# Optimization experiments

Measured on AMD Instinct MI355X. Metric: run time of the kernel, lower is better.

Reference implementation:

```python
import jax, jax.numpy as jnp
import numpy as np

IN_CH = 128
OUT_CH = 1
N_NODES = 20000
N_EDGES = 640000
EPS = 1e-5


def setup_inputs() -> dict:
    key = jax.random.key(0)
    ks = jax.random.split(key, 8)
    x = jax.random.normal(ks[0], (N_NODES, IN_CH), dtype=jnp.float32)
    edge_index = jax.random.randint(ks[1], (2, N_EDGES), 0, N_NODES, dtype=jnp.int64)
    s1 = 1.0 / np.sqrt(2 * IN_CH)
    s2 = 1.0 / np.sqrt(IN_CH)
    return {
        "x": x,
        "edge_index": edge_index,
        "W1": jax.random.normal(ks[2], (2 * IN_CH, IN_CH), dtype=jnp.float32) * s1,
        "b1": jnp.zeros((IN_CH,), dtype=jnp.float32),
        "bn_g": jnp.ones((IN_CH,), dtype=jnp.float32),
        "bn_b": jnp.zeros((IN_CH,), dtype=jnp.float32),
        "W2": jax.random.normal(ks[3], (IN_CH, IN_CH), dtype=jnp.float32) * s2,
        "b2": jnp.zeros((IN_CH,), dtype=jnp.float32),
        "ln_g": jnp.ones((IN_CH,), dtype=jnp.float32),
        "ln_b": jnp.zeros((IN_CH,), dtype=jnp.float32),
        "W3": jax.random.normal(ks[4], (IN_CH, OUT_CH), dtype=jnp.float32) * s2,
        "b3": jnp.zeros((OUT_CH,), dtype=jnp.float32),
    }


def gcn_conv(h, src, dst, num_nodes, bias):
    # h: [num_nodes, F] already linearly transformed. GCN norm with self loops:
    # deg[i] = 1 + in-degree(i); norm_e = deg[src]^-1/2 * deg[dst]^-1/2
    deg = jnp.zeros((num_nodes,), h.dtype).at[dst].add(1.0) + 1.0
    dinv = deg ** -0.5
    norm = dinv[src] * dinv[dst]                      # [E]
    agg = jnp.zeros_like(h).at[dst].add(h[src] * norm[:, None])
    agg = agg + h * (dinv * dinv)[:, None]            # self-loop contribution
    return agg + bias


def reference(x, edge_index, W1, b1, bn_g, bn_b, W2, b2, ln_g, ln_b, W3, b3):
    src, dst = edge_index[0], edge_index[1]
    E = src.shape[0]
    # edge features: [E, 2*IN_CH]
    ef = jnp.concatenate([x[src], x[dst]], axis=1)
    # GCNConv 1 over E "nodes" (edge-feature rows)
    h = gcn_conv(ef @ W1, src, dst, E, b1)
    # BatchNorm1d (training-mode batch stats, biased variance)
    mean = h.mean(axis=0)
    var = h.var(axis=0)
    h = (h - mean) * jax.lax.rsqrt(var + EPS) * bn_g + bn_b
    h = jax.nn.relu(h)
    # GCNConv 2
    h = gcn_conv(h @ W2, src, dst, E, b2)
    # LayerNorm over feature dim
    mu = h.mean(axis=-1, keepdims=True)
    v = h.var(axis=-1, keepdims=True)
    h = (h - mu) * jax.lax.rsqrt(v + EPS) * ln_g + ln_b
    h = jax.nn.relu(h)
    out = h @ W3 + b3                                  # [E, 1]
    return out.squeeze()
```

## Files before the change

kernel.cpp:

```cpp
#include <hip/hip_runtime.h>
#include <hip/hip_bf16.h>

#define NN 20000
#define NE 640000
#define TAILN (NE - NN)
#define F  128
#define EPSN 1e-5f

typedef __bf16 bf16;
typedef bf16  bf16x8 __attribute__((ext_vector_type(8)));
typedef bf16  bf16x4 __attribute__((ext_vector_type(4)));
typedef float f32x4  __attribute__((ext_vector_type(4)));
typedef unsigned short u16;

__global__ void k_cvt_idx(const void* __restrict__ ei_raw, int* __restrict__ srcb,
                          int* __restrict__ dstb, int* __restrict__ cnt,
                          int* __restrict__ cst, int* __restrict__ cdt) {
  const int* e32 = (const int*)ei_raw;
  const long long* e64 = (const long long*)ei_raw;
  bool is64 = true;
#pragma unroll
  for (int k = 0; k < 8; ++k) is64 = is64 && (e32[2 * k + 1] == 0);
  int e = blockIdx.x * 256 + threadIdx.x;
  if (e < NE) {
    int s, d;
    if (is64) { s = (int)e64[e]; d = (int)e64[NE + e]; }
    else      { s = e32[e];      d = e32[NE + e]; }
    srcb[e] = s; dstb[e] = d;
    atomicAdd(&cnt[d], 1);
    if (e >= NN) { atomicAdd(&cst[s], 1); atomicAdd(&cdt[d], 1); }
  }
}

__global__ __launch_bounds__(256) void k1_gemm1(const float* __restrict__ x,
        const float* __restrict__ W1, bf16* __restrict__ xa, bf16* __restrict__ xb) {
  __shared__ float XT[64][129];
  int row0 = blockIdx.x * 64;
  int half = blockIdx.y >> 1;
  int cb   = (blockIdx.y & 1) * 64;
  const float* W = W1 + (size_t)half * F * F;
  bf16* out = half ? xb : xa;
  int t = threadIdx.x;
#pragma unroll
  for (int i = 0; i < 8; ++i) {
    int flat = i * 1024 + t * 4;
    int r = flat >> 7, c = flat & 127;
    int gr = row0 + r;
    f32x4 v = {0.f, 0.f, 0.f, 0.f};
    if (gr < NN) v = *(const f32x4*)(x + (size_t)gr * F + c);
    XT[r][c] = v[0]; XT[r][c + 1] = v[1]; XT[r][c + 2] = v[2]; XT[r][c + 3] = v[3];
  }
  __syncthreads();
  int tc = t & 15, tr = t >> 4;
  float acc[4][4] = {};
  for (int k = 0; k < F; ++k) {
    f32x4 wv = *(const f32x4*)(W + (size_t)k * F + cb + tc * 4);
    float x0 = XT[tr * 4 + 0][k], x1 = XT[tr * 4 + 1][k];
    float x2 = XT[tr * 4 + 2][k], x3 = XT[tr * 4 + 3][k];
#pragma unroll
    for (int j = 0; j < 4; ++j) {
      acc[0][j] += x0 * wv[j]; acc[1][j] += x1 * wv[j];
      acc[2][j] += x2 * wv[j]; acc[3][j] += x3 * wv[j];
    }
  }
#pragma unroll
  for (int i = 0; i < 4; ++i) {
    int gr = row0 + tr * 4 + i;
    if (gr < NN) {
      bf16x4 o;
#pragma unroll
      for (int j = 0; j < 4; ++j) o[j] = (bf16)acc[i][j];
      *(bf16x4*)(out + (size_t)gr * F + cb + tc * 4) = o;
    }
  }
}

__global__ __launch_bounds__(1024) void k3_scan(const int* __restrict__ cnt,
        int* __restrict__ ptr, int* __restrict__ cursor,
        float* __restrict__ dinv, float* __restrict__ invdeg) {
  __shared__ int wsum[16];
  __shared__ int carry_s;
  int t = threadIdx.x;
  int lane = t & 63, wv = t >> 6;
  if (t == 0) carry_s = 0;
  __syncthreads();
  for (int c0 = 0; c0 < NN; c0 += 1024) {
    int i = c0 + t;
    int v = (i < NN) ? cnt[i] : 0;
    int s = v;
#pragma unroll
    for (int off = 1; off < 64; off <<= 1) {
      int n = __shfl_up(s, off);
      if (lane >= off) s += n;
    }
    if (lane == 63) wsum[wv] = s;
    __syncthreads();
    int carry = carry_s;
    int wbase = 0;
#pragma unroll
    for (int k2 = 0; k2 < 16; ++k2) wbase += (k2 < wv) ? wsum[k2] : 0;
    int incl = s + wbase;
    if (i < NN) {
      int excl = carry + incl - v;
      ptr[i] = excl; cursor[i] = excl;
      float deg = (float)(v + 1);
      dinv[i] = rsqrtf(deg);
      invdeg[i] = 1.0f / deg;
    }
    __syncthreads();
    if (t == 1023) carry_s = carry + incl;
    __syncthreads();
  }
  if (t == 0) ptr[NN] = carry_s;
}

__global__ __launch_bounds__(256) void kB_fused(const int* __restrict__ srcb,
        const int* __restrict__ dstb, const bf16* __restrict__ xa,
        const bf16* __restrict__ xb, bf16* __restrict__ hx,
        int* __restrict__ cursor, int* __restrict__ csr_s) {
  int bid = blockIdx.x;
  int t = threadIdx.x;
  if (bid < 2500) {
    int flat = bid * 256 + t;
    int j = flat >> 5, ch = flat & 31;
    if (j >= NN) return;
    if (ch < 16) {
      int s = srcb[j], d = dstb[j];
      bf16x8 a = *(const bf16x8*)(xa + (size_t)s * F + ch * 8);
      bf16x8 b = *(const bf16x8*)(xb + (size_t)d * F + ch * 8);
      bf16x8 o;
#pragma unroll
      for (int m = 0; m < 8; ++m) o[m] = (bf16)((float)a[m] + (float)b[m]);
      *(bf16x8*)(hx + (size_t)j * 256 + ch * 8) = o;
    } else {
      int c8 = (ch - 16) * 8;
      bf16x8 a = *(const bf16x8*)(xa + (size_t)j * F + c8);
      *(bf16x8*)(hx + (size_t)j * 256 + 128 + c8) = a;
    }
  } else {
    int e = (bid - 2500) * 256 + t;
    if (e < NE) {
      int d = dstb[e];
      int pos = atomicAdd(&cursor[d], 1);
      csr_s[pos] = srcb[e] | ((e >= NN) ? (1 << 16) : 0);
    }
  }
}

__global__ __launch_bounds__(256) void k6_conv1cross(const int* __restrict__ ptr,
        const int* __restrict__ csr_s, const bf16* __restrict__ hx,
        const bf16* __restrict__ xb,
        const float* __restrict__ dinv, const float* __restrict__ invdeg,
        const float* __restrict__ b1, float* __restrict__ h1h,
        float* __restrict__ crossrow) {
  int w = threadIdx.x >> 6, lane = threadIdx.x & 63;
  int g = lane >> 4, k = lane & 15;
  int i = blockIdx.x * 4 + w;
  int c0 = k * 8;
  int beg = ptr[i], end = ptr[i + 1];
  float acc[8] = {0,0,0,0,0,0,0,0}, z[8] = {0,0,0,0,0,0,0,0};
  int q = beg + g;
  for (; q + 4 < end; q += 8) {
    int v0 = csr_s[q], v1 = csr_s[q + 4];
    int s0 = v0 & 0xFFFF, s1 = v1 & 0xFFFF;
    float f0 = (v0 >> 16) ? 1.f : 0.f, f1 = (v1 >> 16) ? 1.f : 0.f;
    float d0 = dinv[s0], d1 = dinv[s1];
    const bf16* r0 = hx + (size_t)s0 * 256 + c0;
    const bf16* r1 = hx + (size_t)s1 * 256 + c0;
    bf16x8 h0 = *(const bf16x8*)r0;
    bf16x8 x0 = *(const bf16x8*)(r0 + 128);
    bf16x8 h1 = *(const bf16x8*)r1;
    bf16x8 x1 = *(const bf16x8*)(r1 + 128);
#pragma unroll
    for (int j = 0; j < 8; ++j) {
      acc[j] += d0 * (float)h0[j] + d1 * (float)h1[j];
      z[j]   += f0 * (float)x0[j] + f1 * (float)x1[j];
    }
  }
  if (q < end) {
    int v0 = csr_s[q];
    int s0 = v0 & 0xFFFF;
    float f0 = (v0 >> 16) ? 1.f : 0.f;
    float d0 = dinv[s0];
    const bf16* r0 = hx + (size_t)s0 * 256 + c0;
    bf16x8 h0 = *(const bf16x8*)r0;
    bf16x8 x0 = *(const bf16x8*)(r0 + 128);
#pragma unroll
    for (int j = 0; j < 8; ++j) {
      acc[j] += d0 * (float)h0[j];
      z[j]   += f0 * (float)x0[j];
    }
  }
#pragma unroll
  for (int m = 16; m < 64; m <<= 1) {
#pragma unroll
    for (int j = 0; j < 8; ++j) {
      acc[j] += __shfl_xor(acc[j], m);
      z[j]   += __shfl_xor(z[j], m);
    }
  }
  if (g == 0) {
    float di = dinv[i], iv = invdeg[i];
    bf16x8 self = *(const bf16x8*)(hx + (size_t)i * 256 + c0);
    f32x4 bA = *(const f32x4*)(b1 + c0), bB = *(const f32x4*)(b1 + c0 + 4);
    f32x4 o0, o1;
#pragma unroll
    for (int j = 0; j < 4; ++j) {
      o0[j] = di * acc[j]     + (float)self[j]     * iv + bA[j];
      o1[j] = di * acc[j + 4] + (float)self[j + 4] * iv + bB[j];
    }
    *(f32x4*)(h1h + (size_t)i * F + c0) = o0;
    *(f32x4*)(h1h + (size_t)i * F + c0 + 4) = o1;
  } else if (g == 1) {
    bf16x8 xbv = *(const bf16x8*)(xb + (size_t)i * F + c0);
    f32x4 o0, o1;
#pragma unroll
    for (int j = 0; j < 4; ++j) {
      o0[j] = (float)xbv[j]     * z[j];
      o1[j] = (float)xbv[j + 4] * z[j + 4];
    }
    *(f32x4*)(crossrow + (size_t)i * F + c0) = o0;
    *(f32x4*)(crossrow + (size_t)i * F + c0 + 4) = o1;
  }
}

__global__ __launch_bounds__(256) void k7sr(const float* __restrict__ h1h,
        const float* __restrict__ crossrow, const bf16* __restrict__ xa,
        const bf16* __restrict__ xb, const int* __restrict__ cst,
        const int* __restrict__ cdt, float* __restrict__ statsB) {
  int t = threadIdx.x;
  int w = t >> 6, lane = t & 63, k = lane & 15;
  int rg = t >> 4;
  int c0 = k * 8;
  int base = blockIdx.x * 200;
  float A1[8] = {0,0,0,0,0,0,0,0}, A2[8] = {0,0,0,0,0,0,0,0};
  float B1[8] = {0,0,0,0,0,0,0,0}, B2[8] = {0,0,0,0,0,0,0,0};
  float Cc[8] = {0,0,0,0,0,0,0,0};
  for (int r = rg; r < 200; r += 16) {
    int n = base + r;
    f32x4 h0 = *(const f32x4*)(h1h + (size_t)n * F + c0);
    f32x4 h1 = *(const f32x4*)(h1h + (size_t)n * F + c0 + 4);
    f32x4 cr0 = *(const f32x4*)(crossrow + (size_t)n * F + c0);
    f32x4 cr1 = *(const f32x4*)(crossrow + (size_t)n * F + c0 + 4);
    bf16x8 av = *(const bf16x8*)(xa + (size_t)n * F + c0);
    bf16x8 bv = *(const bf16x8*)(xb + (size_t)n * F + c0);
    float ca = (float)cst[n], cb = (float)cdt[n];
#pragma unroll
    for (int j = 0; j < 4; ++j) {
      A1[j] += h0[j]; A2[j] += h0[j] * h0[j];
      A1[j + 4] += h1[j]; A2[j + 4] += h1[j] * h1[j];
      Cc[j] += cr0[j]; Cc[j + 4] += cr1[j];
    }
#pragma unroll
    for (int j = 0; j < 8; ++j) {
      float a = (float)av[j], b = (float)bv[j];
      B1[j] += ca * a + cb * b;
      B2[j] += ca * a * a + cb * b * b;
    }
  }
#pragma unroll
  for (int m = 16; m < 64; m <<= 1) {
#pragma unroll
    for (int j = 0; j < 8; ++j) {
      A1[j] += __shfl_xor(A1[j], m); A2[j] += __shfl_xor(A2[j], m);
      B1[j] += __shfl_xor(B1[j], m); B2[j] += __shfl_xor(B2[j], m);
      Cc[j] += __shfl_xor(Cc[j], m);
    }
  }
  __shared__ float L[4][5][128];
  if (lane < 16) {
#pragma unroll
    for (int j = 0; j < 8; ++j) {
      L[w][0][c0 + j] = A1[j]; L[w][1][c0 + j] = A2[j];
      L[w][2][c0 + j] = B1[j]; L[w][3][c0 + j] = B2[j];
      L[w][4][c0 + j] = Cc[j];
    }
  }
  __syncthreads();
  if (t < 128) {
#pragma unroll
    for (int term = 0; term < 5; ++term) {
      float v = L[0][term][t] + L[1][term][t] + L[2][term][t] + L[3][term][t];
      atomicAdd(&statsB[term * 128 + t], v);
    }
  }
}

__global__ __launch_bounds__(256) void k8_final(const float* __restrict__ statsB,
        const float* __restrict__ bn_g, const float* __restrict__ bn_b,
        const float* __restrict__ b1, const float* __restrict__ W2,
        const float* __restrict__ b2, const float* __restrict__ lng,
        const float* __restrict__ lnb, const float* __restrict__ W3,
        float* __restrict__ P, float* __restrict__ Qh, float* __restrict__ Qt,
        u16* __restrict__ W2t, f32x4* __restrict__ params4) {
  int t = threadIdx.x;
  if (t < 128) {
    float A1 = statsB[t], A2 = statsB[128 + t], B1v = statsB[256 + t];
    float B2v = statsB[384 + t], Cv = statsB[512 + t];
    float b1c = b1[t];
    float S = A1 + B1v + (float)TAILN * b1c;
    float Q = A2 + B2v + 2.f * Cv + 2.f * b1c * B1v + (float)TAILN * b1c * b1c;
    float mean = S * (1.0f / NE);
    float var = Q * (1.0f / NE) - mean * mean;
    float rs = rsqrtf(var + EPSN);
    float p = bn_g[t] * rs;
    float sh = bn_b[t] - mean * p;
    P[t] = p; Qh[t] = sh; Qt[t] = p * b1c + sh;
    f32x4 pr = {b2[t], lng[t], lnb[t], W3[t]};
    params4[t] = pr;
  }
  for (int i = 0; i < 64; ++i) {
    int flat = i * 256 + t;
    int k = flat >> 7, c = flat & 127;
    union { bf16 b; u16 u; } cv;
    cv.b = (bf16)W2[(size_t)k * F + c];
    W2t[(size_t)c * F + k] = cv.u;
  }
}

__global__ __launch_bounds__(256) void k9a_headgemm(const float* __restrict__ h1h,
        const float* __restrict__ P, const float* __restrict__ Qh,
        const u16* __restrict__ W2t, bf16* __restrict__ h2ph) {
  __shared__ __align__(16) bf16 A[64 * 128];
  __shared__ __align__(16) bf16 B[128 * 128];
  int t = threadIdx.x;
  int row0 = blockIdx.x * 64;
  const bf16x8* srcB = (const bf16x8*)W2t;
#pragma unroll
  for (int i = 0; i < 8; ++i) {
    int ch = i * 256 + t;
    int r = ch >> 4, cir = ch & 15;
    *(bf16x8*)&B[r * 128 + ((cir ^ (r & 7)) << 3)] = srcB[ch];
  }
  {
    int r = t >> 2, sub = t & 3;
    int gr = row0 + r;
#pragma unroll
    for (int j = 0; j < 4; ++j) {
      int c0 = sub * 32 + j * 8;
      f32x4 v0 = {0.f,0.f,0.f,0.f}, v1 = {0.f,0.f,0.f,0.f};
      if (gr < NN) {
        v0 = *(const f32x4*)(h1h + (size_t)gr * F + c0);
        v1 = *(const f32x4*)(h1h + (size_t)gr * F + c0 + 4);
      }
      f32x4 p0 = *(const f32x4*)(P + c0), p1 = *(const f32x4*)(P + c0 + 4);
      f32x4 q0 = *(const f32x4*)(Qh + c0), q1 = *(const f32x4*)(Qh + c0 + 4);
      bf16x8 o;
#pragma unroll
      for (int m = 0; m < 4; ++m) {
        o[m]     = (bf16)fmaxf(v0[m] * p0[m] + q0[m], 0.f);
        o[m + 4] = (bf16)fmaxf(v1[m] * p1[m] + q1[m], 0.f);
      }
      int ch = c0 >> 3;
      *(bf16x8*)&A[r * 128 + ((ch ^ (r & 7)) << 3)] = o;
    }
  }
  __syncthreads();
  int lane = t & 63, w = t >> 6;
  int lr = lane & 15, g = lane >> 4;
  int arow = w * 16 + lr;
  bf16x8 af[4];
#pragma unroll
  for (int kk = 0; kk < 4; ++kk)
    af[kk] = *(const bf16x8*)&A[arow * 128 + (((kk * 4 + g) ^ (arow & 7)) << 3)];
  f32x4 acc[8];
#pragma unroll
  for (int n = 0; n < 8; ++n) {
    f32x4 a = {0.f,0.f,0.f,0.f};
    int col = n * 16 + lr;
#pragma unroll
    for (int kk = 0; kk < 4; ++kk) {
      bf16x8 bfr = *(const bf16x8*)&B[col * 128 + (((kk * 4 + g) ^ (col & 7)) << 3)];
      a = __builtin_amdgcn_mfma_f32_16x16x32_bf16(af[kk], bfr, a, 0, 0, 0);
    }
    acc[n] = a;
  }
#pragma unroll
  for (int n = 0; n < 8; ++n) {
#pragma unroll
    for (int r4 = 0; r4 < 4; ++r4) {
      int gr = row0 + w * 16 + g * 4 + r4;
      if (gr < NN) h2ph[(size_t)gr * F + n * 16 + lr] = (bf16)acc[n][r4];
    }
  }
}

__global__ __launch_bounds__(256) void k9b_head(const int* __restrict__ ptr,
        const int* __restrict__ csr_s, const bf16* __restrict__ h2ph,
        const float* __restrict__ dinv, const float* __restrict__ invdeg,
        const float* __restrict__ b2, const float* __restrict__ lng,
        const float* __restrict__ lnb, const float* __restrict__ W3,
        const float* __restrict__ b3, float* __restrict__ out) {
  int w = threadIdx.x >> 6, lane = threadIdx.x & 63;
  int g = lane >> 4, k = lane & 15;
  int i = blockIdx.x * 4 + w;
  int c0 = k * 8;
  int beg = ptr[i], end = ptr[i + 1];
  float acc[8] = {0,0,0,0,0,0,0,0};
  int q = beg + g;
  for (; q + 4 < end; q += 8) {
    int s0 = csr_s[q] & 0xFFFF, s1 = csr_s[q + 4] & 0xFFFF;
    float d0 = dinv[s0], d1 = dinv[s1];
    bf16x8 h0 = *(const bf16x8*)(h2ph + (size_t)s0 * F + c0);
    bf16x8 h1 = *(const bf16x8*)(h2ph + (size_t)s1 * F + c0);
#pragma unroll
    for (int j = 0; j < 8; ++j)
      acc[j] += d0 * (float)h0[j] + d1 * (float)h1[j];
  }
  if (q < end) {
    int s0 = csr_s[q] & 0xFFFF;
    float d0 = dinv[s0];
    bf16x8 h0 = *(const bf16x8*)(h2ph + (size_t)s0 * F + c0);
#pragma unroll
    for (int j = 0; j < 8; ++j) acc[j] += d0 * (float)h0[j];
  }
#pragma unroll
  for (int m = 16; m < 64; m <<= 1) {
#pragma unroll
    for (int j = 0; j < 8; ++j) acc[j] += __shfl_xor(acc[j], m);
  }
  float di = dinv[i], iv = invdeg[i];
  bf16x8 self = *(const bf16x8*)(h2ph + (size_t)i * F + c0);
  f32x4 b2A = *(const f32x4*)(b2 + c0), b2B = *(const f32x4*)(b2 + c0 + 4);
  float h2[8];
#pragma unroll
  for (int j = 0; j < 4; ++j) {
    h2[j]     = di * acc[j]     + (float)self[j]     * iv + b2A[j];
    h2[j + 4] = di * acc[j + 4] + (float)self[j + 4] * iv + b2B[j];
  }
  float s1v = 0.f, s2v = 0.f;
#pragma unroll
  for (int j = 0; j < 8; ++j) { s1v += h2[j]; s2v += h2[j] * h2[j]; }
#pragma unroll
  for (int m = 1; m < 16; m <<= 1) { s1v += __shfl_xor(s1v, m); s2v += __shfl_xor(s2v, m); }
  float mean = s1v * (1.0f / F);
  float var = s2v * (1.0f / F) - mean * mean;
  float rs = rsqrtf(var + EPSN);
  f32x4 lgA = *(const f32x4*)(lng + c0), lgB = *(const f32x4*)(lng + c0 + 4);
  f32x4 lbA = *(const f32x4*)(lnb + c0), lbB = *(const f32x4*)(lnb + c0 + 4);
  f32x4 w3A = *(const f32x4*)(W3 + c0),  w3B = *(const f32x4*)(W3 + c0 + 4);
  float y = 0.f;
#pragma unroll
  for (int j = 0; j < 4; ++j) {
    y += fmaxf((h2[j]     - mean) * rs * lgA[j] + lbA[j], 0.f) * w3A[j];
    y += fmaxf((h2[j + 4] - mean) * rs * lgB[j] + lbB[j], 0.f) * w3B[j];
  }
#pragma unroll
  for (int m = 1; m < 16; m <<= 1) y += __shfl_xor(y, m);
  if (lane == 0) out[i] = y + b3[0];
}

__global__ __launch_bounds__(256) void k9c_tail(const int* __restrict__ srcb,
        const int* __restrict__ dstb, const bf16* __restrict__ xa,
        const bf16* __restrict__ xb, const float* __restrict__ P,
        const float* __restrict__ Qt, const u16* __restrict__ W2t,
        const f32x4* __restrict__ params4, const float* __restrict__ b3,
        float* __restrict__ out) {
  __shared__ __align__(16) bf16 B[128 * 128];
  int t = threadIdx.x;
  const bf16x8* srcB = (const bf16x8*)W2t;
#pragma unroll
  for (int i = 0; i < 8; ++i) {
    int ch = i * 256 + t;
    int r = ch >> 4, cir = ch & 15;
    *(bf16x8*)&B[r * 128 + ((cir ^ (r & 7)) << 3)] = srcB[ch];
  }
  __syncthreads();
  int lane = t & 63, w = t >> 6;
  int lr = lane & 15, g = lane >> 4;
  int ebase = NN + blockIdx.x * 256 + w * 64;
  float b3v = b3[0];
  for (int rc = 0; rc < 4; ++rc) {
    int e = ebase + rc * 16 + lr;
    bool ok = (e < NE);
    int se = 0, de = 0;
    if (ok) { se = srcb[e]; de = dstb[e]; }
    bf16x8 af[4];
#pragma unroll
    for (int kk = 0; kk < 4; ++kk) {
      int c0 = kk * 32 + g * 8;
      bf16x8 o;
      if (ok) {
        bf16x8 av = *(const bf16x8*)(xa + (size_t)se * F + c0);
        bf16x8 bv = *(const bf16x8*)(xb + (size_t)de * F + c0);
        f32x4 p0 = *(const f32x4*)(P + c0), p1 = *(const f32x4*)(P + c0 + 4);
        f32x4 q0 = *(const f32x4*)(Qt + c0), q1 = *(const f32x4*)(Qt + c0 + 4);
#pragma unroll
        for (int m = 0; m < 4; ++m) {
          o[m]     = (bf16)fmaxf(((float)av[m] + (float)bv[m]) * p0[m] + q0[m], 0.f);
          o[m + 4] = (bf16)fmaxf(((float)av[m + 4] + (float)bv[m + 4]) * p1[m] + q1[m], 0.f);
        }
      } else {
#pragma unroll
        for (int m = 0; m < 8; ++m) o[m] = (bf16)0.f;
      }
      af[kk] = o;
    }
    f32x4 acc[8];
#pragma unroll
    for (int n = 0; n < 8; ++n) {
      f32x4 a = {0.f,0.f,0.f,0.f};
      int col = n * 16 + lr;
#pragma unroll
      for (int kk = 0; kk < 4; ++kk) {
        bf16x8 bfr = *(const bf16x8*)&B[col * 128 + (((kk * 4 + g) ^ (col & 7)) << 3)];
        a = __builtin_amdgcn_mfma_f32_16x16x32_bf16(af[kk], bfr, a, 0, 0, 0);
      }
      acc[n] = a;
    }
#pragma unroll
    for (int r4 = 0; r4 < 4; ++r4) {
      float vv[8];
      float s = 0.f, q = 0.f;
#pragma unroll
      for (int n = 0; n < 8; ++n) {
        float v = acc[n][r4] + params4[n * 16 + lr][0];
        vv[n] = v; s += v; q += v * v;
      }
#pragma unroll
      for (int m = 1; m < 16; m <<= 1) { s += __shfl_xor(s, m); q += __shfl_xor(q, m); }
      float mean = s * (1.0f / F);
      float var = q * (1.0f / F) - mean * mean;
      float rs = rsqrtf(var + EPSN);
      float o = 0.f;
#pragma unroll
      for (int n = 0; n < 8; ++n) {
        f32x4 pr = params4[n * 16 + lr];
        o += fmaxf((vv[n] - mean) * rs * pr[1] + pr[2], 0.f) * pr[3];
      }
#pragma unroll
      for (int m = 1; m < 16; m <<= 1) o += __shfl_xor(o, m);
      int eo = ebase + rc * 16 + g * 4 + r4;
      if (lr == 0 && eo < NE) out[eo] = o + b3v;
    }
  }
}

extern "C" void kernel_launch(void* const* d_in, const int* in_sizes, int n_in,
                              void* d_out, int out_size, void* d_ws, size_t ws_size,
                              hipStream_t stream) {
  const float* x   = (const float*)d_in[0];
  const void*  ei  = d_in[1];
  const float* W1  = (const float*)d_in[2];
  const float* b1  = (const float*)d_in[3];
  const float* bng = (const float*)d_in[4];
  const float* bnb = (const float*)d_in[5];
  const float* W2  = (const float*)d_in[6];
  const float* b2  = (const float*)d_in[7];
  const float* lng = (const float*)d_in[8];
  const float* lnb = (const float*)d_in[9];
  const float* W3  = (const float*)d_in[10];
  const float* b3  = (const float*)d_in[11];
  float* out = (float*)d_out;

  char* ws = (char*)d_ws;
  size_t off = 0;
  auto alloc = [&](size_t bytes) -> char* {
    off = (off + 511) & ~(size_t)511;
    char* p = ws + off;
    off += bytes;
    return p;
  };
  const size_t NFh = (size_t)NN * F * 2;
  bf16*  xa     = (bf16*)alloc(NFh);
  bf16*  xb     = (bf16*)alloc(NFh);
  bf16*  hx     = (bf16*)alloc((size_t)NN * 256 * 2);
  float* h1h    = (float*)alloc((size_t)NN * F * 4);
  float* crossr = (float*)alloc((size_t)NN * F * 4);
  int*   srcb   = (int*)alloc((size_t)NE * 4);
  int*   dstb   = (int*)alloc((size_t)NE * 4);
  int*   csr_s  = (int*)alloc((size_t)NE * 4);
  int*   cnt    = (int*)alloc((size_t)NN * 4);
  int*   cst    = (int*)alloc((size_t)NN * 4);
  int*   cdt    = (int*)alloc((size_t)NN * 4);
  int*   ptrb   = (int*)alloc((size_t)(NN + 1) * 4);
  int*   cursor = (int*)alloc((size_t)NN * 4);
  float* dinv   = (float*)alloc((size_t)NN * 4);
  float* invdeg = (float*)alloc((size_t)NN * 4);
  float* statsB = (float*)alloc(5 * 128 * 4);
  float* Pp     = (float*)alloc(128 * 4);
  float* Qh     = (float*)alloc(128 * 4);
  float* Qt     = (float*)alloc(128 * 4);
  u16*   W2t    = (u16*)alloc((size_t)F * F * 2);
  f32x4* params4= (f32x4*)alloc(128 * 16);
  bf16*  h2ph   = hx;

  hipMemsetAsync(cnt, 0, (size_t)NN * 4, stream);
  hipMemsetAsync(cst, 0, (size_t)NN * 4, stream);
  hipMemsetAsync(cdt, 0, (size_t)NN * 4, stream);
  hipMemsetAsync(statsB, 0, 5 * 128 * 4, stream);

  k_cvt_idx<<<2500, 256, 0, stream>>>(ei, srcb, dstb, cnt, cst, cdt);
  k1_gemm1<<<dim3(313, 4), 256, 0, stream>>>(x, W1, xa, xb);
  k3_scan<<<1, 1024, 0, stream>>>(cnt, ptrb, cursor, dinv, invdeg);
  kB_fused<<<5000, 256, 0, stream>>>(srcb, dstb, xa, xb, hx, cursor, csr_s);
  k6_conv1cross<<<5000, 256, 0, stream>>>(ptrb, csr_s, hx, xb, dinv, invdeg, b1,
                                          h1h, crossr);
  k7sr<<<100, 256, 0, stream>>>(h1h, crossr, xa, xb, cst, cdt, statsB);
  k8_final<<<1, 256, 0, stream>>>(statsB, bng, bnb, b1, W2, b2, lng, lnb, W3,
                                  Pp, Qh, Qt, W2t, params4);
  k9a_headgemm<<<313, 256, 0, stream>>>(h1h, Pp, Qh, W2t, h2ph);
  k9b_head<<<5000, 256, 0, stream>>>(ptrb, csr_s, h2ph, dinv, invdeg, b2, lng, lnb,
                                     W3, b3, out);
  k9c_tail<<<2422, 256, 0, stream>>>(srcb, dstb, xa, xb, Pp, Qt, W2t, params4,
                                     b3, out);
}
```

Before: 459.5 us.

## Prescale rows by dinv and fuse head aggregation with tail kernel

Multiplies each source row by dinv when hx and g2 are written, so the aggregation loops no longer gather dinv[s] per edge and the self-loop term collapses to di*(acc+self). The k9b head aggregation and k9c tail MFMA kernels are merged into one launch that branches on block index, so the two independent workloads can run concurrently and one launch disappears. In exchange, the prescaled values are rounded to bf16 after scaling, which changes the numerics slightly. Tail blocks now carry the extra parameter and register footprint of the fused kernel, and a launch-bounds occupancy hint is added.

```diff
diff --git a/kernel.cpp b/kernel.cpp
--- a/kernel.cpp
+++ b/kernel.cpp
@@ -116,8 +116,8 @@
 
 __global__ __launch_bounds__(256) void kB_fused(const int* __restrict__ srcb,
         const int* __restrict__ dstb, const bf16* __restrict__ xa,
-        const bf16* __restrict__ xb, bf16* __restrict__ hx,
-        int* __restrict__ cursor, int* __restrict__ csr_s) {
+        const bf16* __restrict__ xb, const float* __restrict__ dinv,
+        bf16* __restrict__ hx, int* __restrict__ cursor, int* __restrict__ csr_s) {
   int bid = blockIdx.x;
   int t = threadIdx.x;
   if (bid < 2500) {
@@ -126,11 +126,12 @@
     if (j >= NN) return;
     if (ch < 16) {
       int s = srcb[j], d = dstb[j];
+      float dj = dinv[j];
       bf16x8 a = *(const bf16x8*)(xa + (size_t)s * F + ch * 8);
       bf16x8 b = *(const bf16x8*)(xb + (size_t)d * F + ch * 8);
       bf16x8 o;
 #pragma unroll
-      for (int m = 0; m < 8; ++m) o[m] = (bf16)((float)a[m] + (float)b[m]);
+      for (int m = 0; m < 8; ++m) o[m] = (bf16)(dj * ((float)a[m] + (float)b[m]));
       *(bf16x8*)(hx + (size_t)j * 256 + ch * 8) = o;
     } else {
       int c8 = (ch - 16) * 8;
@@ -150,7 +151,7 @@
 __global__ __launch_bounds__(256) void k6_conv1cross(const int* __restrict__ ptr,
         const int* __restrict__ csr_s, const bf16* __restrict__ hx,
         const bf16* __restrict__ xb,
-        const float* __restrict__ dinv, const float* __restrict__ invdeg,
+        const float* __restrict__ dinv,
         const float* __restrict__ b1, float* __restrict__ h1h,
         float* __restrict__ crossrow) {
   int w = threadIdx.x >> 6, lane = threadIdx.x & 63;
@@ -164,7 +165,6 @@
     int v0 = csr_s[q], v1 = csr_s[q + 4];
     int s0 = v0 & 0xFFFF, s1 = v1 & 0xFFFF;
     float f0 = (v0 >> 16) ? 1.f : 0.f, f1 = (v1 >> 16) ? 1.f : 0.f;
-    float d0 = dinv[s0], d1 = dinv[s1];
     const bf16* r0 = hx + (size_t)s0 * 256 + c0;
     const bf16* r1 = hx + (size_t)s1 * 256 + c0;
     bf16x8 h0 = *(const bf16x8*)r0;
@@ -173,7 +173,7 @@
     bf16x8 x1 = *(const bf16x8*)(r1 + 128);
 #pragma unroll
     for (int j = 0; j < 8; ++j) {
-      acc[j] += d0 * (float)h0[j] + d1 * (float)h1[j];
+      acc[j] += (float)h0[j] + (float)h1[j];
       z[j]   += f0 * (float)x0[j] + f1 * (float)x1[j];
     }
   }
@@ -181,13 +181,12 @@
     int v0 = csr_s[q];
     int s0 = v0 & 0xFFFF;
     float f0 = (v0 >> 16) ? 1.f : 0.f;
-    float d0 = dinv[s0];
     const bf16* r0 = hx + (size_t)s0 * 256 + c0;
     bf16x8 h0 = *(const bf16x8*)r0;
     bf16x8 x0 = *(const bf16x8*)(r0 + 128);
 #pragma unroll
     for (int j = 0; j < 8; ++j) {
-      acc[j] += d0 * (float)h0[j];
+      acc[j] += (float)h0[j];
       z[j]   += f0 * (float)x0[j];
     }
   }
@@ -200,14 +199,14 @@
     }
   }
   if (g == 0) {
-    float di = dinv[i], iv = invdeg[i];
+    float di = dinv[i];
     bf16x8 self = *(const bf16x8*)(hx + (size_t)i * 256 + c0);
     f32x4 bA = *(const f32x4*)(b1 + c0), bB = *(const f32x4*)(b1 + c0 + 4);
     f32x4 o0, o1;
 #pragma unroll
     for (int j = 0; j < 4; ++j) {
-      o0[j] = di * acc[j]     + (float)self[j]     * iv + bA[j];
-      o1[j] = di * acc[j + 4] + (float)self[j + 4] * iv + bB[j];
+      o0[j] = di * (acc[j]     + (float)self[j])     + bA[j];
+      o1[j] = di * (acc[j + 4] + (float)self[j + 4]) + bB[j];
     }
     *(f32x4*)(h1h + (size_t)i * F + c0) = o0;
     *(f32x4*)(h1h + (size_t)i * F + c0 + 4) = o1;
@@ -320,7 +319,8 @@
 
 __global__ __launch_bounds__(256) void k9a_headgemm(const float* __restrict__ h1h,
         const float* __restrict__ P, const float* __restrict__ Qh,
-        const u16* __restrict__ W2t, bf16* __restrict__ h2ph) {
+        const u16* __restrict__ W2t, const float* __restrict__ dinv,
+        bf16* __restrict__ g2) {
   __shared__ __align__(16) bf16 A[64 * 128];
   __shared__ __align__(16) bf16 B[128 * 128];
   int t = threadIdx.x;
@@ -376,163 +376,162 @@
     acc[n] = a;
   }
 #pragma unroll
-  for (int n = 0; n < 8; ++n) {
-#pragma unroll
-    for (int r4 = 0; r4 < 4; ++r4) {
-      int gr = row0 + w * 16 + g * 4 + r4;
-      if (gr < NN) h2ph[(size_t)gr * F + n * 16 + lr] = (bf16)acc[n][r4];
-    }
-  }
-}
-
-__global__ __launch_bounds__(256) void k9b_head(const int* __restrict__ ptr,
-        const int* __restrict__ csr_s, const bf16* __restrict__ h2ph,
-        const float* __restrict__ dinv, const float* __restrict__ invdeg,
-        const float* __restrict__ b2, const float* __restrict__ lng,
-        const float* __restrict__ lnb, const float* __restrict__ W3,
-        const float* __restrict__ b3, float* __restrict__ out) {
-  int w = threadIdx.x >> 6, lane = threadIdx.x & 63;
-  int g = lane >> 4, k = lane & 15;
-  int i = blockIdx.x * 4 + w;
-  int c0 = k * 8;
-  int beg = ptr[i], end = ptr[i + 1];
-  float acc[8] = {0,0,0,0,0,0,0,0};
-  int q = beg + g;
-  for (; q + 4 < end; q += 8) {
-    int s0 = csr_s[q] & 0xFFFF, s1 = csr_s[q + 4] & 0xFFFF;
-    float d0 = dinv[s0], d1 = dinv[s1];
-    bf16x8 h0 = *(const bf16x8*)(h2ph + (size_t)s0 * F + c0);
-    bf16x8 h1 = *(const bf16x8*)(h2ph + (size_t)s1 * F + c0);
-#pragma unroll
-    for (int j = 0; j < 8; ++j)
-      acc[j] += d0 * (float)h0[j] + d1 * (float)h1[j];
-  }
-  if (q < end) {
-    int s0 = csr_s[q] & 0xFFFF;
-    float d0 = dinv[s0];
-    bf16x8 h0 = *(const bf16x8*)(h2ph + (size_t)s0 * F + c0);
-#pragma unroll
-    for (int j = 0; j < 8; ++j) acc[j] += d0 * (float)h0[j];
-  }
-#pragma unroll
-  for (int m = 16; m < 64; m <<= 1) {
-#pragma unroll
-    for (int j = 0; j < 8; ++j) acc[j] += __shfl_xor(acc[j], m);
-  }
-  float di = dinv[i], iv = invdeg[i];
-  bf16x8 self = *(const bf16x8*)(h2ph + (size_t)i * F + c0);
-  f32x4 b2A = *(const f32x4*)(b2 + c0), b2B = *(const f32x4*)(b2 + c0 + 4);
-  float h2[8];
-#pragma unroll
-  for (int j = 0; j < 4; ++j) {
-    h2[j]     = di * acc[j]     + (float)self[j]     * iv + b2A[j];
-    h2[j + 4] = di * acc[j + 4] + (float)self[j + 4] * iv + b2B[j];
-  }
-  float s1v = 0.f, s2v = 0.f;
-#pragma unroll
-  for (int j = 0; j < 8; ++j) { s1v += h2[j]; s2v += h2[j] * h2[j]; }
-#pragma unroll
-  for (int m = 1; m < 16; m <<= 1) { s1v += __shfl_xor(s1v, m); s2v += __shfl_xor(s2v, m); }
-  float mean = s1v * (1.0f / F);
-  float var = s2v * (1.0f / F) - mean * mean;
-  float rs = rsqrtf(var + EPSN);
-  f32x4 lgA = *(const f32x4*)(lng + c0), lgB = *(const f32x4*)(lng + c0 + 4);
-  f32x4 lbA = *(const f32x4*)(lnb + c0), lbB = *(const f32x4*)(lnb + c0 + 4);
-  f32x4 w3A = *(const f32x4*)(W3 + c0),  w3B = *(const f32x4*)(W3 + c0 + 4);
-  float y = 0.f;
-#pragma unroll
-  for (int j = 0; j < 4; ++j) {
-    y += fmaxf((h2[j]     - mean) * rs * lgA[j] + lbA[j], 0.f) * w3A[j];
-    y += fmaxf((h2[j + 4] - mean) * rs * lgB[j] + lbB[j], 0.f) * w3B[j];
-  }
-#pragma unroll
-  for (int m = 1; m < 16; m <<= 1) y += __shfl_xor(y, m);
-  if (lane == 0) out[i] = y + b3[0];
-}
-
-__global__ __launch_bounds__(256) void k9c_tail(const int* __restrict__ srcb,
+  for (int r4 = 0; r4 < 4; ++r4) {
+    int gr = row0 + w * 16 + g * 4 + r4;
+    if (gr < NN) {
+      float dr = dinv[gr];
+#pragma unroll
+      for (int n = 0; n < 8; ++n)
+        g2[(size_t)gr * F + n * 16 + lr] = (bf16)(acc[n][r4] * dr);
+    }
+  }
+}
+
+__global__ __launch_bounds__(256, 4) void kC_fused(const int* __restrict__ srcb,
         const int* __restrict__ dstb, const bf16* __restrict__ xa,
         const bf16* __restrict__ xb, const float* __restrict__ P,
         const float* __restrict__ Qt, const u16* __restrict__ W2t,
         const f32x4* __restrict__ params4, const float* __restrict__ b3,
+        const int* __restrict__ ptr, const int* __restrict__ csr_s,
+        const bf16* __restrict__ g2, const float* __restrict__ dinv,
+        const float* __restrict__ b2, const float* __restrict__ lng,
+        const float* __restrict__ lnb, const float* __restrict__ W3,
         float* __restrict__ out) {
   __shared__ __align__(16) bf16 B[128 * 128];
+  int bid = blockIdx.x;
   int t = threadIdx.x;
-  const bf16x8* srcB = (const bf16x8*)W2t;
-#pragma unroll
-  for (int i = 0; i < 8; ++i) {
-    int ch = i * 256 + t;
-    int r = ch >> 4, cir = ch & 15;
-    *(bf16x8*)&B[r * 128 + ((cir ^ (r & 7)) << 3)] = srcB[ch];
-  }
-  __syncthreads();
   int lane = t & 63, w = t >> 6;
-  int lr = lane & 15, g = lane >> 4;
-  int ebase = NN + blockIdx.x * 256 + w * 64;
-  float b3v = b3[0];
-  for (int rc = 0; rc < 4; ++rc) {
-    int e = ebase + rc * 16 + lr;
-    bool ok = (e < NE);
-    int se = 0, de = 0;
-    if (ok) { se = srcb[e]; de = dstb[e]; }
-    bf16x8 af[4];
-#pragma unroll
-    for (int kk = 0; kk < 4; ++kk) {
-      int c0 = kk * 32 + g * 8;
-      bf16x8 o;
-      if (ok) {
-        bf16x8 av = *(const bf16x8*)(xa + (size_t)se * F + c0);
-        bf16x8 bv = *(const bf16x8*)(xb + (size_t)de * F + c0);
-        f32x4 p0 = *(const f32x4*)(P + c0), p1 = *(const f32x4*)(P + c0 + 4);
-        f32x4 q0 = *(const f32x4*)(Qt + c0), q1 = *(const f32x4*)(Qt + c0 + 4);
-#pragma unroll
-        for (int m = 0; m < 4; ++m) {
-          o[m]     = (bf16)fmaxf(((float)av[m] + (float)bv[m]) * p0[m] + q0[m], 0.f);
-          o[m + 4] = (bf16)fmaxf(((float)av[m + 4] + (float)bv[m + 4]) * p1[m] + q1[m], 0.f);
+  if (bid < 2422) {
+    const bf16x8* srcB = (const bf16x8*)W2t;
+#pragma unroll
+    for (int i = 0; i < 8; ++i) {
+      int ch = i * 256 + t;
+      int r = ch >> 4, cir = ch & 15;
+      *(bf16x8*)&B[r * 128 + ((cir ^ (r & 7)) << 3)] = srcB[ch];
+    }
+    __syncthreads();
+    int lr = lane & 15, g = lane >> 4;
+    int ebase = NN + bid * 256 + w * 64;
+    float b3v = b3[0];
+    for (int rc = 0; rc < 4; ++rc) {
+      int e = ebase + rc * 16 + lr;
+      bool ok = (e < NE);
+      int se = 0, de = 0;
+      if (ok) { se = srcb[e]; de = dstb[e]; }
+      bf16x8 af[4];
+#pragma unroll
+      for (int kk = 0; kk < 4; ++kk) {
+        int c0 = kk * 32 + g * 8;
+        bf16x8 o;
+        if (ok) {
+          bf16x8 av = *(const bf16x8*)(xa + (size_t)se * F + c0);
+          bf16x8 bv = *(const bf16x8*)(xb + (size_t)de * F + c0);
+          f32x4 p0 = *(const f32x4*)(P + c0), p1 = *(const f32x4*)(P + c0 + 4);
+          f32x4 q0 = *(const f32x4*)(Qt + c0), q1 = *(const f32x4*)(Qt + c0 + 4);
+#pragma unroll
+          for (int m = 0; m < 4; ++m) {
+            o[m]     = (bf16)fmaxf(((float)av[m] + (float)bv[m]) * p0[m] + q0[m], 0.f);
+            o[m + 4] = (bf16)fmaxf(((float)av[m + 4] + (float)bv[m + 4]) * p1[m] + q1[m], 0.f);
+          }
+        } else {
+#pragma unroll
+          for (int m = 0; m < 8; ++m) o[m] = (bf16)0.f;
         }
-      } else {
-#pragma unroll
-        for (int m = 0; m < 8; ++m) o[m] = (bf16)0.f;
+        af[kk] = o;
       }
-      af[kk] = o;
-    }
-    f32x4 acc[8];
-#pragma unroll
-    for (int n = 0; n < 8; ++n) {
-      f32x4 a = {0.f,0.f,0.f,0.f};
-      int col = n * 16 + lr;
-#pragma unroll
-      for (int kk = 0; kk < 4; ++kk) {
-        bf16x8 bfr = *(const bf16x8*)&B[col * 128 + (((kk * 4 + g) ^ (col & 7)) << 3)];
-        a = __builtin_amdgcn_mfma_f32_16x16x32_bf16(af[kk], bfr, a, 0, 0, 0);
+      f32x4 acc[8];
+#pragma unroll
+      for (int n = 0; n < 8; ++n) {
+        f32x4 a = {0.f,0.f,0.f,0.f};
+        int col = n * 16 + lr;
+#pragma unroll
+        for (int kk = 0; kk < 4; ++kk) {
+          bf16x8 bfr = *(const bf16x8*)&B[col * 128 + (((kk * 4 + g) ^ (col & 7)) << 3)];
+          a = __builtin_amdgcn_mfma_f32_16x16x32_bf16(af[kk], bfr, a, 0, 0, 0);
+        }
+        acc[n] = a;
       }
-      acc[n] = a;
-    }
-#pragma unroll
-    for (int r4 = 0; r4 < 4; ++r4) {
-      float vv[8];
-      float s = 0.f, q = 0.f;
-#pragma unroll
-      for (int n = 0; n < 8; ++n) {
-        float v = acc[n][r4] + params4[n * 16 + lr][0];
-        vv[n] = v; s += v; q += v * v;
+#pragma unroll
+      for (int r4 = 0; r4 < 4; ++r4) {
+        float vv[8];
+        float s = 0.f, q = 0.f;
+#pragma unroll
+        for (int n = 0; n < 8; ++n) {
+          float v = acc[n][r4] + params4[n * 16 + lr][0];
+          vv[n] = v; s += v; q += v * v;
+        }
+#pragma unroll
+        for (int m = 1; m < 16; m <<= 1) { s += __shfl_xor(s, m); q += __shfl_xor(q, m); }
+        float mean = s * (1.0f / F);
+        float var = q * (1.0f / F) - mean * mean;
+        float rs = rsqrtf(var + EPSN);
+        float o = 0.f;
+#pragma unroll
+        for (int n = 0; n < 8; ++n) {
+          f32x4 pr = params4[n * 16 + lr];
+          o += fmaxf((vv[n] - mean) * rs * pr[1] + pr[2], 0.f) * pr[3];
+        }
+#pragma unroll
+        for (int m = 1; m < 16; m <<= 1) o += __shfl_xor(o, m);
+        int eo = ebase + rc * 16 + g * 4 + r4;
+        if (lr == 0 && eo < NE) out[eo] = o + b3v;
       }
-#pragma unroll
-      for (int m = 1; m < 16; m <<= 1) { s += __shfl_xor(s, m); q += __shfl_xor(q, m); }
-      float mean = s * (1.0f / F);
-      float var = q * (1.0f / F) - mean * mean;
-      float rs = rsqrtf(var + EPSN);
-      float o = 0.f;
-#pragma unroll
-      for (int n = 0; n < 8; ++n) {
-        f32x4 pr = params4[n * 16 + lr];
-        o += fmaxf((vv[n] - mean) * rs * pr[1] + pr[2], 0.f) * pr[3];
-      }
-#pragma unroll
-      for (int m = 1; m < 16; m <<= 1) o += __shfl_xor(o, m);
-      int eo = ebase + rc * 16 + g * 4 + r4;
-      if (lr == 0 && eo < NE) out[eo] = o + b3v;
-    }
+    }
+  } else {
+    int g = lane >> 4, k = lane & 15;
+    int i = (bid - 2422) * 4 + w;
+    int c0 = k * 8;
+    int beg = ptr[i], end = ptr[i + 1];
+    float acc[8] = {0,0,0,0,0,0,0,0};
+    int q = beg + g;
+    for (; q + 4 < end; q += 8) {
+      int s0 = csr_s[q] & 0xFFFF, s1 = csr_s[q + 4] & 0xFFFF;
+      bf16x8 h0 = *(const bf16x8*)(g2 + (size_t)s0 * F + c0);
+      bf16x8 h1 = *(const bf16x8*)(g2 + (size_t)s1 * F + c0);
+#pragma unroll
+      for (int j = 0; j < 8; ++j)
+        acc[j] += (float)h0[j] + (float)h1[j];
+    }
+    if (q < end) {
+      int s0 = csr_s[q] & 0xFFFF;
+      bf16x8 h0 = *(const bf16x8*)(g2 + (size_t)s0 * F + c0);
+#pragma unroll
+      for (int j = 0; j < 8; ++j) acc[j] += (float)h0[j];
+    }
+#pragma unroll
+    for (int m = 16; m < 64; m <<= 1) {
+#pragma unroll
+      for (int j = 0; j < 8; ++j) acc[j] += __shfl_xor(acc[j], m);
+    }
+    float di = dinv[i];
+    bf16x8 self = *(const bf16x8*)(g2 + (size_t)i * F + c0);
+    f32x4 b2A = *(const f32x4*)(b2 + c0), b2B = *(const f32x4*)(b2 + c0 + 4);
+    float h2[8];
+#pragma unroll
+    for (int j = 0; j < 4; ++j) {
+      h2[j]     = di * (acc[j]     + (float)self[j])     + b2A[j];
+      h2[j + 4] = di * (acc[j + 4] + (float)self[j + 4]) + b2B[j];
+    }
+    float s1v = 0.f, s2v = 0.f;
+#pragma unroll
+    for (int j = 0; j < 8; ++j) { s1v += h2[j]; s2v += h2[j] * h2[j]; }
+#pragma unroll
+    for (int m = 1; m < 16; m <<= 1) { s1v += __shfl_xor(s1v, m); s2v += __shfl_xor(s2v, m); }
+    float mean = s1v * (1.0f / F);
+    float var = s2v * (1.0f / F) - mean * mean;
+    float rs = rsqrtf(var + EPSN);
+    f32x4 lgA = *(const f32x4*)(lng + c0), lgB = *(const f32x4*)(lng + c0 + 4);
+    f32x4 lbA = *(const f32x4*)(lnb + c0), lbB = *(const f32x4*)(lnb + c0 + 4);
+    f32x4 w3A = *(const f32x4*)(W3 + c0),  w3B = *(const f32x4*)(W3 + c0 + 4);
+    float y = 0.f;
+#pragma unroll
+    for (int j = 0; j < 4; ++j) {
+      y += fmaxf((h2[j]     - mean) * rs * lgA[j] + lbA[j], 0.f) * w3A[j];
+      y += fmaxf((h2[j + 4] - mean) * rs * lgB[j] + lbB[j], 0.f) * w3B[j];
+    }
+#pragma unroll
+    for (int m = 1; m < 16; m <<= 1) y += __shfl_xor(y, m);
+    if (lane == 0) out[i] = y + b3[0];
   }
 }
 
@@ -583,7 +582,7 @@
   float* Qt     = (float*)alloc(128 * 4);
   u16*   W2t    = (u16*)alloc((size_t)F * F * 2);
   f32x4* params4= (f32x4*)alloc(128 * 16);
-  bf16*  h2ph   = hx;
+  bf16*  g2     = hx;
 
   hipMemsetAsync(cnt, 0, (size_t)NN * 4, stream);
   hipMemsetAsync(cst, 0, (size_t)NN * 4, stream);
@@ -593,15 +592,12 @@
   k_cvt_idx<<<2500, 256, 0, stream>>>(ei, srcb, dstb, cnt, cst, cdt);
   k1_gemm1<<<dim3(313, 4), 256, 0, stream>>>(x, W1, xa, xb);
   k3_scan<<<1, 1024, 0, stream>>>(cnt, ptrb, cursor, dinv, invdeg);
-  kB_fused<<<5000, 256, 0, stream>>>(srcb, dstb, xa, xb, hx, cursor, csr_s);
-  k6_conv1cross<<<5000, 256, 0, stream>>>(ptrb, csr_s, hx, xb, dinv, invdeg, b1,
-                                          h1h, crossr);
+  kB_fused<<<5000, 256, 0, stream>>>(srcb, dstb, xa, xb, dinv, hx, cursor, csr_s);
+  k6_conv1cross<<<5000, 256, 0, stream>>>(ptrb, csr_s, hx, xb, dinv, b1, h1h, crossr);
   k7sr<<<100, 256, 0, stream>>>(h1h, crossr, xa, xb, cst, cdt, statsB);
   k8_final<<<1, 256, 0, stream>>>(statsB, bng, bnb, b1, W2, b2, lng, lnb, W3,
                                   Pp, Qh, Qt, W2t, params4);
-  k9a_headgemm<<<313, 256, 0, stream>>>(h1h, Pp, Qh, W2t, h2ph);
-  k9b_head<<<5000, 256, 0, stream>>>(ptrb, csr_s, h2ph, dinv, invdeg, b2, lng, lnb,
-                                     W3, b3, out);
-  k9c_tail<<<2422, 256, 0, stream>>>(srcb, dstb, xa, xb, Pp, Qt, W2t, params4,
-                                     b3, out);
-}
+  k9a_headgemm<<<313, 256, 0, stream>>>(h1h, Pp, Qh, W2t, dinv, g2);
+  kC_fused<<<7422, 256, 0, stream>>>(srcb, dstb, xa, xb, Pp, Qt, W2t, params4, b3,
+                                     ptrb, csr_s, g2, dinv, b2, lng, lnb, W3, out);
+}
```

After: 566.4 us. +23.3%, slower.
